# Performance work log

Measured on AMD Instinct MI355X. Metric: run time of the kernel, lower is better.

The kernel has to match this reference:

```python
import jax, jax.numpy as jnp
import numpy as np

B, C, H, W = 8, 256, 48, 48
EPS = 1e-5  # BatchNorm2d default eps


def setup_inputs() -> dict:
    key = jax.random.key(0)
    ks = jax.random.split(key, 8)
    return {
        "Q_feat_s": jax.random.normal(ks[0], (B, C, H, W), dtype=jnp.float32),
        "KV_feat_s": jax.random.normal(ks[1], (B, C, H, W), dtype=jnp.float32),
        "Wq": jax.random.normal(ks[2], (C, C), dtype=jnp.float32) * 0.02,
        "Wk": jax.random.normal(ks[3], (C, C), dtype=jnp.float32) * 0.02,
        "Wv": jax.random.normal(ks[4], (C, C), dtype=jnp.float32) * 0.02,
        "Wz": jax.random.normal(ks[5], (C, C), dtype=jnp.float32) * 0.02,
        "bn_gamma": jnp.ones((C,), dtype=jnp.float32),
        "bn_beta": jnp.zeros((C,), dtype=jnp.float32),
        "bn_mean": jax.random.normal(ks[6], (C,), dtype=jnp.float32) * 0.1,
        "bn_var": jax.random.uniform(ks[7], (C,), dtype=jnp.float32, minval=0.5, maxval=1.5),
    }


def reference(Q_feat_s, KV_feat_s, Wq, Wk, Wv, Wz, bn_gamma, bn_beta, bn_mean, bn_var):
    b, c, h, w = Q_feat_s.shape
    n = h * w
    # 1x1 convs == channel-mixing matmuls
    Q = jnp.einsum('oc,bchw->bohw', Wq, Q_feat_s).reshape(b, c, n)      # [B,C,N]
    K = jnp.einsum('oc,bchw->bohw', Wk, KV_feat_s).reshape(b, c, n)     # [B,C,N]
    V = jnp.einsum('oc,bchw->bohw', Wv, KV_feat_s).reshape(b, c, n)     # [B,C,N]
    # attn = (Q^T K)/N then @ V^T; linear (no softmax) so reassociate: Q^T (K V^T)/N
    KV = jnp.einsum('bcn,bdn->bcd', K, V) / n                           # [B,C,C]
    QKV = jnp.einsum('bcn,bcd->bdn', Q, KV)                             # [B,C,N]
    x = QKV.reshape(b, c, h, w)
    # W_z 1x1 conv + BatchNorm2d (inference / running stats)
    z = jnp.einsum('oc,bchw->bohw', Wz, x)
    inv = bn_gamma / jnp.sqrt(bn_var + EPS)
    z = z * inv[None, :, None, None] + (bn_beta - bn_mean * inv)[None, :, None, None]
    return z + Q_feat_s
```

## Files before the change

### kernel.cpp

```cpp
#include <hip/hip_runtime.h>

#define Bv 8
#define Cc 256
#define Nn 2304
#define EPS 1e-5f

typedef float f32x4 __attribute__((ext_vector_type(4)));
typedef __bf16 bf16x8 __attribute__((ext_vector_type(8)));

static __device__ __forceinline__ f32x4 mfma16(bf16x8 a, bf16x8 b, f32x4 c) {
    return __builtin_amdgcn_mfma_f32_16x16x32_bf16(a, b, c, 0, 0, 0);
}

static __device__ __forceinline__ bf16x8 load_cvt8(const float* __restrict__ p) {
    float4 a = *(const float4*)p;
    float4 b = *(const float4*)(p + 4);
    bf16x8 r;
    r[0] = (__bf16)a.x; r[1] = (__bf16)a.y; r[2] = (__bf16)a.z; r[3] = (__bf16)a.w;
    r[4] = (__bf16)b.x; r[5] = (__bf16)b.y; r[6] = (__bf16)b.z; r[7] = (__bf16)b.w;
    return r;
}

static __device__ __forceinline__ bf16x8 load_add_cvt8(const float* __restrict__ p0,
                                                       const float* __restrict__ p1) {
    float4 a0 = *(const float4*)p0;
    float4 a1 = *(const float4*)(p0 + 4);
    float4 b0 = *(const float4*)p1;
    float4 b1 = *(const float4*)(p1 + 4);
    bf16x8 r;
    r[0] = (__bf16)(a0.x + b0.x); r[1] = (__bf16)(a0.y + b0.y);
    r[2] = (__bf16)(a0.z + b0.z); r[3] = (__bf16)(a0.w + b0.w);
    r[4] = (__bf16)(a1.x + b1.x); r[5] = (__bf16)(a1.y + b1.y);
    r[6] = (__bf16)(a1.z + b1.z); r[7] = (__bf16)(a1.w + b1.w);
    return r;
}

__global__ __launch_bounds__(256) void k_fused1(
    const float* __restrict__ Qf, const float* __restrict__ KVf,
    const float* __restrict__ Wq, const float* __restrict__ Wk,
    const float* __restrict__ Wv, const float* __restrict__ Wz,
    const float* __restrict__ gamma, const float* __restrict__ var_,
    unsigned short* __restrict__ Lb_us, unsigned short* __restrict__ Rtb_us,
    unsigned short* __restrict__ Qft_us, float* __restrict__ Spart) {
    __shared__ __align__(16) char smem[32768];
    int blk = blockIdx.x, tid = threadIdx.x;

    if (blk < 256) {
        __bf16 (*As)[72] = (__bf16 (*)[72])smem;
        __bf16 (*Bs)[72] = (__bf16 (*)[72])(smem + 9216);
        int b = blk & 7;
        int tt = (blk >> 3) & 15;
        int kc = blk >> 7;
        int tr = (tt >> 2) * 64, tc = (tt & 3) * 64;
        int k0 = kc * 1152;
        int l = tid & 63, w = tid >> 6;
        int lr = l & 15, kofs = (l >> 4) * 8;
        int row = tid >> 2, c0 = (tid & 3) * 16;
        const float* Abase = KVf + ((size_t)b * Cc + tr) * Nn + k0;
        const float* Bbase = KVf + ((size_t)b * Cc + tc) * Nn + k0;
        f32x4 zero = {0.f, 0.f, 0.f, 0.f};
        f32x4 acc[4] = {zero, zero, zero, zero};
        for (int ks = 0; ks < 18; ++ks) {
            const float* ap = Abase + (size_t)row * Nn + ks * 64 + c0;
            const float* bp = Bbase + (size_t)row * Nn + ks * 64 + c0;
            *(bf16x8*)&As[row][c0]     = load_cvt8(ap);
            *(bf16x8*)&As[row][c0 + 8] = load_cvt8(ap + 8);
            *(bf16x8*)&Bs[row][c0]     = load_cvt8(bp);
            *(bf16x8*)&Bs[row][c0 + 8] = load_cvt8(bp + 8);
            __syncthreads();
#pragma unroll
            for (int kk = 0; kk < 64; kk += 32) {
                bf16x8 af = *(const bf16x8*)&As[w * 16 + lr][kk + kofs];
#pragma unroll
                for (int j = 0; j < 4; ++j) {
                    bf16x8 bb = *(const bf16x8*)&Bs[j * 16 + lr][kk + kofs];
                    acc[j] = mfma16(af, bb, acc[j]);
                }
            }
            __syncthreads();
        }
        float* Sp = Spart + ((size_t)kc * Bv + b) * 65536;
        int row0 = tr + w * 16 + ((l >> 4) << 2);
#pragma unroll
        for (int j = 0; j < 4; ++j) {
            int col = tc + j * 16 + lr;
#pragma unroll
            for (int r = 0; r < 4; ++r)
                Sp[(size_t)(row0 + r) * 256 + col] = acc[j][r];
        }
    } else if (blk < 768) {
        float* bufA = (float*)smem;
        float* bufB = bufA + 4096;
        __bf16* Lb  = (__bf16*)Lb_us;
        __bf16* Rtb = (__bf16*)Rtb_us;
        int wblk = blk - 256;
        bool isL = (wblk < 256);
        int t = isL ? wblk : wblk - 256;
        int tr = (t >> 4) * 16, tc = (t & 15) * 16;
        if (isL) {
            for (int idx = tid; idx < 4096; idx += 256) {
                int r = idx >> 8, m = idx & 255;
                bufA[idx] = Wz[(tr + r) * 256 + m];
            }
            for (int idx = tid; idx < 4096; idx += 256) {
                int m = idx >> 4, j = idx & 15;
                bufB[idx] = Wv[m * 256 + tc + j];
            }
        } else {
            for (int idx = tid; idx < 4096; idx += 256) {
                int o = idx >> 4, j = idx & 15;
                bufA[idx] = Wq[o * 256 + tr + j];
                bufB[idx] = Wk[o * 256 + tc + j];
            }
        }
        __syncthreads();
        int oo = tid >> 4, cc = tid & 15;
        float sum = 0.f;
        if (isL) {
#pragma unroll 8
            for (int m = 0; m < 256; ++m) sum += bufA[oo * 256 + m] * bufB[m * 16 + cc];
            int o = tr + oo;
            float inv = gamma[o] / sqrtf(var_[o] + EPS);
            Lb[o * 256 + tc + cc] = (__bf16)(inv * sum * (1.0f / (float)Nn));
        } else {
#pragma unroll 8
            for (int o = 0; o < 256; ++o) sum += bufA[o * 16 + oo] * bufB[o * 16 + cc];
            Rtb[(tr + oo) * 256 + tc + cc] = (__bf16)sum;
        }
    } else {
        float (*tile)[65] = (float (*)[65])smem;
        __bf16* Qft = (__bf16*)Qft_us;
        int t = blk - 768;
        int c0 = (t & 3) * 64;
        int u = t >> 2;
        int n0 = (u % 36) * 64;
        int b = u / 36;
        const float* src = Qf + (size_t)b * Cc * Nn;
        for (int idx = tid; idx < 4096; idx += 256) {
            int r = idx >> 6, cl = idx & 63;
            tile[r][cl] = src[(size_t)(c0 + r) * Nn + n0 + cl];
        }
        __syncthreads();
        __bf16* dst = Qft + ((size_t)b * Nn + n0) * 256 + c0;
        for (int idx = tid; idx < 4096; idx += 256) {
            int n = idx >> 6, c = idx & 63;
            dst[(size_t)n * 256 + c] = (__bf16)tile[c][n];
        }
    }
}

__global__ __launch_bounds__(256) void k_mid1(
    const unsigned short* __restrict__ Lb_us, const float* __restrict__ Spart,
    float* __restrict__ Tpart) {
    const __bf16* Lb = (const __bf16*)Lb_us;
    int blk = blockIdx.x;
    int b = blk & 7;
    int t = (blk >> 3) & 15;
    int kc = blk >> 7;
    int tr = (t >> 2) * 64, tc = (t & 3) * 64;
    int k0 = kc * 128;
    int tid = threadIdx.x, l = tid & 63, w = tid >> 6;
    int lr = l & 15, kofs = (l >> 4) * 8;
    const float* S0 = Spart + (size_t)b * 65536;
    const float* S1 = Spart + (size_t)(Bv + b) * 65536;
    f32x4 zero = {0.f, 0.f, 0.f, 0.f};
    f32x4 acc[4] = {zero, zero, zero, zero};
    int arow = tr + w * 16 + lr;
    for (int kk = 0; kk < 128; kk += 32) {
        bf16x8 af = *(const bf16x8*)&Lb[arow * 256 + k0 + kk + kofs];
#pragma unroll
        for (int j = 0; j < 4; ++j) {
            int brow = tc + j * 16 + lr;
            bf16x8 bb = load_add_cvt8(&S0[(size_t)brow * 256 + k0 + kk + kofs],
                                      &S1[(size_t)brow * 256 + k0 + kk + kofs]);
            acc[j] = mfma16(af, bb, acc[j]);
        }
    }
    float* Tp = Tpart + ((size_t)kc * Bv + b) * 65536;
    int row0 = tr + w * 16 + ((l >> 4) << 2);
#pragma unroll
    for (int j = 0; j < 4; ++j) {
        int col = tc + j * 16 + lr;
#pragma unroll
        for (int r = 0; r < 4; ++r)
            Tp[(size_t)(row0 + r) * 256 + col] = acc[j][r];
    }
}

__global__ __launch_bounds__(256) void k_mid2(
    const float* __restrict__ Tpart, const unsigned short* __restrict__ Rtb_us,
    unsigned short* __restrict__ Pb_us) {
    const __bf16* Rtb = (const __bf16*)Rtb_us;
    __bf16* Pb = (__bf16*)Pb_us;
    int blk = blockIdx.x;
    int b = blk & 7;
    int t = blk >> 3;
    int tr = (t >> 2) * 64, tc = (t & 3) * 64;
    int tid = threadIdx.x, l = tid & 63, w = tid >> 6;
    int lr = l & 15, kofs = (l >> 4) * 8;
    const float* T0 = Tpart + (size_t)b * 65536;
    const float* T1 = Tpart + (size_t)(Bv + b) * 65536;
    f32x4 zero = {0.f, 0.f, 0.f, 0.f};
    f32x4 acc[4] = {zero, zero, zero, zero};
    int arow = tr + w * 16 + lr;
    for (int kk = 0; kk < 256; kk += 32) {
        bf16x8 af = load_add_cvt8(&T0[(size_t)arow * 256 + kk + kofs],
                                  &T1[(size_t)arow * 256 + kk + kofs]);
#pragma unroll
        for (int j = 0; j < 4; ++j) {
            int brow = tc + j * 16 + lr;
            bf16x8 bb = *(const bf16x8*)&Rtb[brow * 256 + kk + kofs];
            acc[j] = mfma16(af, bb, acc[j]);
        }
    }
    __bf16* Pbb = Pb + ((size_t)b << 16);
    int row0 = tr + w * 16 + ((l >> 4) << 2);
#pragma unroll
    for (int j = 0; j < 4; ++j) {
        int col = tc + j * 16 + lr;
#pragma unroll
        for (int r = 0; r < 4; ++r)
            Pbb[(size_t)(row0 + r) * 256 + col] = (__bf16)acc[j][r];
    }
}

__global__ __launch_bounds__(512) void k_out(
    const unsigned short* __restrict__ Pb_us, const unsigned short* __restrict__ Qft_us,
    const float* __restrict__ Qf,
    const float* __restrict__ gamma, const float* __restrict__ beta,
    const float* __restrict__ mean, const float* __restrict__ var_,
    float* __restrict__ out) {
    const __bf16* Pb = (const __bf16*)Pb_us;
    const __bf16* Qft = (const __bf16*)Qft_us;
    int bid = blockIdx.x;
    int b = bid & 7, nt = bid >> 3;
    int tid = threadIdx.x, l = tid & 63, w = tid >> 6;
    int lr = l & 15, kofs = (l >> 4) * 8;
    int obase = w * 32;
    int nbase = nt * 64;
    const __bf16* A = Pb + ((size_t)b << 16);
    const __bf16* Bt = Qft + (size_t)b * Nn * 256;
    f32x4 zero = {0.f, 0.f, 0.f, 0.f};
    f32x4 acc[2][4];
#pragma unroll
    for (int i = 0; i < 2; ++i)
#pragma unroll
        for (int j = 0; j < 4; ++j) acc[i][j] = zero;

    for (int kk = 0; kk < 256; kk += 32) {
        bf16x8 af[2], bb[4];
#pragma unroll
        for (int i = 0; i < 2; ++i)
            af[i] = *(const bf16x8*)&A[(size_t)(obase + i * 16 + lr) * 256 + kk + kofs];
#pragma unroll
        for (int j = 0; j < 4; ++j)
            bb[j] = *(const bf16x8*)&Bt[(size_t)(nbase + j * 16 + lr) * 256 + kk + kofs];
#pragma unroll
        for (int i = 0; i < 2; ++i)
#pragma unroll
            for (int j = 0; j < 4; ++j)
                acc[i][j] = mfma16(af[i], bb[j], acc[i][j]);
    }

    const float* Qfb = Qf + (size_t)b * Cc * Nn;
    float* outb = out + (size_t)b * Cc * Nn;
#pragma unroll
    for (int i = 0; i < 2; ++i) {
        int o0 = obase + i * 16 + ((l >> 4) << 2);
#pragma unroll
        for (int r = 0; r < 4; ++r) {
            int o = o0 + r;
            float inv = gamma[o] / sqrtf(var_[o] + EPS);
            float shift = beta[o] - mean[o] * inv;
#pragma unroll
            for (int j = 0; j < 4; ++j) {
                int n = nbase + j * 16 + lr;
                outb[(size_t)o * Nn + n] = acc[i][j][r] + shift + Qfb[(size_t)o * Nn + n];
            }
        }
    }
}

extern "C" void kernel_launch(void* const* d_in, const int* in_sizes, int n_in,
                              void* d_out, int out_size, void* d_ws, size_t ws_size,
                              hipStream_t stream) {
    (void)in_sizes; (void)n_in; (void)out_size; (void)ws_size;
    const float* Qf    = (const float*)d_in[0];
    const float* KVf   = (const float*)d_in[1];
    const float* Wq    = (const float*)d_in[2];
    const float* Wk    = (const float*)d_in[3];
    const float* Wv    = (const float*)d_in[4];
    const float* Wz    = (const float*)d_in[5];
    const float* gamma = (const float*)d_in[6];
    const float* beta  = (const float*)d_in[7];
    const float* mean  = (const float*)d_in[8];
    const float* var_  = (const float*)d_in[9];
    float* out = (float*)d_out;

    char* ws = (char*)d_ws;
    float* Spart        = (float*)ws;
    float* Tpart        = (float*)(ws + (4u << 20));
    unsigned short* Lb  = (unsigned short*)(ws + (8u << 20));
    unsigned short* Rtb = (unsigned short*)(ws + (8u << 20) + (128u << 10));
    unsigned short* Pb  = (unsigned short*)(ws + (8u << 20) + (256u << 10));
    unsigned short* Qft = (unsigned short*)(ws + (9u << 20) + (256u << 10));

    k_fused1<<<1920, 256, 0, stream>>>(Qf, KVf, Wq, Wk, Wv, Wz, gamma, var_,
                                       Lb, Rtb, Qft, Spart);
    k_mid1<<<256, 256, 0, stream>>>(Lb, Spart, Tpart);
    k_mid2<<<128, 256, 0, stream>>>(Tpart, Rtb, Pb);
    k_out<<<288, 512, 0, stream>>>(Pb, Qft, Qf, gamma, beta, mean, var_, out);
}
```

Before: 165.3 us.

## Fuse Q transpose into output kernel, split Gram K-reduction four ways, prefetch tiles

Drops the separate Q-feature transpose/bf16 conversion stage and its workspace round-trip. The output GEMM kernel now loads the fp32 Q tile, converts it and transposes it into shared memory directly. The KV Gram computation is split into four K-chunks instead of two, doubling the block count for better occupancy, with register prefetch of the next tile overlapping the MFMA work. The mid kernel now sums four partials instead of two, which adds partial-buffer traffic. Shared-memory transposed stores in k_out may bank-conflict.

```diff
diff --git a/kernel.cpp b/kernel.cpp
--- a/kernel.cpp
+++ b/kernel.cpp
@@ -12,12 +12,33 @@
     return __builtin_amdgcn_mfma_f32_16x16x32_bf16(a, b, c, 0, 0, 0);
 }
 
-static __device__ __forceinline__ bf16x8 load_cvt8(const float* __restrict__ p) {
-    float4 a = *(const float4*)p;
-    float4 b = *(const float4*)(p + 4);
+static __device__ __forceinline__ bf16x8 cvt8(float4 a, float4 b) {
     bf16x8 r;
     r[0] = (__bf16)a.x; r[1] = (__bf16)a.y; r[2] = (__bf16)a.z; r[3] = (__bf16)a.w;
     r[4] = (__bf16)b.x; r[5] = (__bf16)b.y; r[6] = (__bf16)b.z; r[7] = (__bf16)b.w;
+    return r;
+}
+
+static __device__ __forceinline__ bf16x8 load_cvt8(const float* __restrict__ p) {
+    return cvt8(*(const float4*)p, *(const float4*)(p + 4));
+}
+
+static __device__ __forceinline__ bf16x8 load4_add_cvt8(
+    const float* __restrict__ p0, const float* __restrict__ p1,
+    const float* __restrict__ p2, const float* __restrict__ p3) {
+    float4 x0 = *(const float4*)p0, x1 = *(const float4*)(p0 + 4);
+    float4 y0 = *(const float4*)p1, y1 = *(const float4*)(p1 + 4);
+    float4 z0 = *(const float4*)p2, z1 = *(const float4*)(p2 + 4);
+    float4 w0 = *(const float4*)p3, w1 = *(const float4*)(p3 + 4);
+    bf16x8 r;
+    r[0] = (__bf16)(x0.x + y0.x + z0.x + w0.x);
+    r[1] = (__bf16)(x0.y + y0.y + z0.y + w0.y);
+    r[2] = (__bf16)(x0.z + y0.z + z0.z + w0.z);
+    r[3] = (__bf16)(x0.w + y0.w + z0.w + w0.w);
+    r[4] = (__bf16)(x1.x + y1.x + z1.x + w1.x);
+    r[5] = (__bf16)(x1.y + y1.y + z1.y + w1.y);
+    r[6] = (__bf16)(x1.z + y1.z + z1.z + w1.z);
+    r[7] = (__bf16)(x1.w + y1.w + z1.w + w1.w);
     return r;
 }
 
@@ -35,39 +56,48 @@
     return r;
 }
 
-__global__ __launch_bounds__(256) void k_fused1(
-    const float* __restrict__ Qf, const float* __restrict__ KVf,
+__global__ __launch_bounds__(256) void k_front(
+    const float* __restrict__ KVf,
     const float* __restrict__ Wq, const float* __restrict__ Wk,
     const float* __restrict__ Wv, const float* __restrict__ Wz,
     const float* __restrict__ gamma, const float* __restrict__ var_,
     unsigned short* __restrict__ Lb_us, unsigned short* __restrict__ Rtb_us,
-    unsigned short* __restrict__ Qft_us, float* __restrict__ Spart) {
+    float* __restrict__ Spart) {
     __shared__ __align__(16) char smem[32768];
     int blk = blockIdx.x, tid = threadIdx.x;
 
-    if (blk < 256) {
+    if (blk < 512) {
         __bf16 (*As)[72] = (__bf16 (*)[72])smem;
         __bf16 (*Bs)[72] = (__bf16 (*)[72])(smem + 9216);
         int b = blk & 7;
         int tt = (blk >> 3) & 15;
         int kc = blk >> 7;
         int tr = (tt >> 2) * 64, tc = (tt & 3) * 64;
-        int k0 = kc * 1152;
+        int k0 = kc * 576;
         int l = tid & 63, w = tid >> 6;
         int lr = l & 15, kofs = (l >> 4) * 8;
         int row = tid >> 2, c0 = (tid & 3) * 16;
-        const float* Abase = KVf + ((size_t)b * Cc + tr) * Nn + k0;
-        const float* Bbase = KVf + ((size_t)b * Cc + tc) * Nn + k0;
+        const float* Ap = KVf + ((size_t)b * Cc + tr + row) * Nn + k0 + c0;
+        const float* Bp = KVf + ((size_t)b * Cc + tc + row) * Nn + k0 + c0;
+        float4 fa0, fa1, fa2, fa3, fb0, fb1, fb2, fb3;
+#define LD_TILE(ks) do { \
+        const float* ap_ = Ap + (ks) * 64; \
+        const float* bp_ = Bp + (ks) * 64; \
+        fa0 = *(const float4*)ap_;         fa1 = *(const float4*)(ap_ + 4); \
+        fa2 = *(const float4*)(ap_ + 8);   fa3 = *(const float4*)(ap_ + 12); \
+        fb0 = *(const float4*)bp_;         fb1 = *(const float4*)(bp_ + 4); \
+        fb2 = *(const float4*)(bp_ + 8);   fb3 = *(const float4*)(bp_ + 12); \
+    } while (0)
         f32x4 zero = {0.f, 0.f, 0.f, 0.f};
         f32x4 acc[4] = {zero, zero, zero, zero};
-        for (int ks = 0; ks < 18; ++ks) {
-            const float* ap = Abase + (size_t)row * Nn + ks * 64 + c0;
-            const float* bp = Bbase + (size_t)row * Nn + ks * 64 + c0;
-            *(bf16x8*)&As[row][c0]     = load_cvt8(ap);
-            *(bf16x8*)&As[row][c0 + 8] = load_cvt8(ap + 8);
-            *(bf16x8*)&Bs[row][c0]     = load_cvt8(bp);
-            *(bf16x8*)&Bs[row][c0 + 8] = load_cvt8(bp + 8);
+        LD_TILE(0);
+        for (int ks = 0; ks < 9; ++ks) {
+            *(bf16x8*)&As[row][c0]     = cvt8(fa0, fa1);
+            *(bf16x8*)&As[row][c0 + 8] = cvt8(fa2, fa3);
+            *(bf16x8*)&Bs[row][c0]     = cvt8(fb0, fb1);
+            *(bf16x8*)&Bs[row][c0 + 8] = cvt8(fb2, fb3);
             __syncthreads();
+            if (ks < 8) LD_TILE(ks + 1);
 #pragma unroll
             for (int kk = 0; kk < 64; kk += 32) {
                 bf16x8 af = *(const bf16x8*)&As[w * 16 + lr][kk + kofs];
@@ -79,6 +109,7 @@
             }
             __syncthreads();
         }
+#undef LD_TILE
         float* Sp = Spart + ((size_t)kc * Bv + b) * 65536;
         int row0 = tr + w * 16 + ((l >> 4) << 2);
 #pragma unroll
@@ -88,12 +119,12 @@
             for (int r = 0; r < 4; ++r)
                 Sp[(size_t)(row0 + r) * 256 + col] = acc[j][r];
         }
-    } else if (blk < 768) {
+    } else {
         float* bufA = (float*)smem;
         float* bufB = bufA + 4096;
         __bf16* Lb  = (__bf16*)Lb_us;
         __bf16* Rtb = (__bf16*)Rtb_us;
-        int wblk = blk - 256;
+        int wblk = blk - 512;
         bool isL = (wblk < 256);
         int t = isL ? wblk : wblk - 256;
         int tr = (t >> 4) * 16, tc = (t & 15) * 16;
@@ -127,25 +158,6 @@
             for (int o = 0; o < 256; ++o) sum += bufA[o * 16 + oo] * bufB[o * 16 + cc];
             Rtb[(tr + oo) * 256 + tc + cc] = (__bf16)sum;
         }
-    } else {
-        float (*tile)[65] = (float (*)[65])smem;
-        __bf16* Qft = (__bf16*)Qft_us;
-        int t = blk - 768;
-        int c0 = (t & 3) * 64;
-        int u = t >> 2;
-        int n0 = (u % 36) * 64;
-        int b = u / 36;
-        const float* src = Qf + (size_t)b * Cc * Nn;
-        for (int idx = tid; idx < 4096; idx += 256) {
-            int r = idx >> 6, cl = idx & 63;
-            tile[r][cl] = src[(size_t)(c0 + r) * Nn + n0 + cl];
-        }
-        __syncthreads();
-        __bf16* dst = Qft + ((size_t)b * Nn + n0) * 256 + c0;
-        for (int idx = tid; idx < 4096; idx += 256) {
-            int n = idx >> 6, c = idx & 63;
-            dst[(size_t)n * 256 + c] = (__bf16)tile[c][n];
-        }
     }
 }
 
@@ -161,8 +173,10 @@
     int k0 = kc * 128;
     int tid = threadIdx.x, l = tid & 63, w = tid >> 6;
     int lr = l & 15, kofs = (l >> 4) * 8;
-    const float* S0 = Spart + (size_t)b * 65536;
-    const float* S1 = Spart + (size_t)(Bv + b) * 65536;
+    const float* S0 = Spart + (size_t)(0 * Bv + b) * 65536;
+    const float* S1 = Spart + (size_t)(1 * Bv + b) * 65536;
+    const float* S2 = Spart + (size_t)(2 * Bv + b) * 65536;
+    const float* S3 = Spart + (size_t)(3 * Bv + b) * 65536;
     f32x4 zero = {0.f, 0.f, 0.f, 0.f};
     f32x4 acc[4] = {zero, zero, zero, zero};
     int arow = tr + w * 16 + lr;
@@ -170,9 +184,8 @@
         bf16x8 af = *(const bf16x8*)&Lb[arow * 256 + k0 + kk + kofs];
 #pragma unroll
         for (int j = 0; j < 4; ++j) {
-            int brow = tc + j * 16 + lr;
-            bf16x8 bb = load_add_cvt8(&S0[(size_t)brow * 256 + k0 + kk + kofs],
-                                      &S1[(size_t)brow * 256 + k0 + kk + kofs]);
+            size_t boff = (size_t)(tc + j * 16 + lr) * 256 + k0 + kk + kofs;
+            bf16x8 bb = load4_add_cvt8(S0 + boff, S1 + boff, S2 + boff, S3 + boff);
             acc[j] = mfma16(af, bb, acc[j]);
         }
     }
@@ -225,21 +238,31 @@
 }
 
 __global__ __launch_bounds__(512) void k_out(
-    const unsigned short* __restrict__ Pb_us, const unsigned short* __restrict__ Qft_us,
-    const float* __restrict__ Qf,
+    const unsigned short* __restrict__ Pb_us, const float* __restrict__ Qf,
     const float* __restrict__ gamma, const float* __restrict__ beta,
     const float* __restrict__ mean, const float* __restrict__ var_,
     float* __restrict__ out) {
+    __shared__ __bf16 Qs[64][264];
     const __bf16* Pb = (const __bf16*)Pb_us;
-    const __bf16* Qft = (const __bf16*)Qft_us;
     int bid = blockIdx.x;
     int b = bid & 7, nt = bid >> 3;
+    int n0 = nt * 64;
     int tid = threadIdx.x, l = tid & 63, w = tid >> 6;
     int lr = l & 15, kofs = (l >> 4) * 8;
+
+    const float* src = Qf + (size_t)b * Cc * Nn + n0;
+    for (int idx = tid; idx < 4096; idx += 512) {
+        int c = idx >> 4, ng = (idx & 15) << 2;
+        float4 v = *(const float4*)(src + (size_t)c * Nn + ng);
+        Qs[ng + 0][c] = (__bf16)v.x;
+        Qs[ng + 1][c] = (__bf16)v.y;
+        Qs[ng + 2][c] = (__bf16)v.z;
+        Qs[ng + 3][c] = (__bf16)v.w;
+    }
+    __syncthreads();
+
     int obase = w * 32;
-    int nbase = nt * 64;
     const __bf16* A = Pb + ((size_t)b << 16);
-    const __bf16* Bt = Qft + (size_t)b * Nn * 256;
     f32x4 zero = {0.f, 0.f, 0.f, 0.f};
     f32x4 acc[2][4];
 #pragma unroll
@@ -254,7 +277,7 @@
             af[i] = *(const bf16x8*)&A[(size_t)(obase + i * 16 + lr) * 256 + kk + kofs];
 #pragma unroll
         for (int j = 0; j < 4; ++j)
-            bb[j] = *(const bf16x8*)&Bt[(size_t)(nbase + j * 16 + lr) * 256 + kk + kofs];
+            bb[j] = *(const bf16x8*)&Qs[j * 16 + lr][kk + kofs];
 #pragma unroll
         for (int i = 0; i < 2; ++i)
 #pragma unroll
@@ -274,7 +297,7 @@
             float shift = beta[o] - mean[o] * inv;
 #pragma unroll
             for (int j = 0; j < 4; ++j) {
-                int n = nbase + j * 16 + lr;
+                int n = n0 + j * 16 + lr;
                 outb[(size_t)o * Nn + n] = acc[i][j][r] + shift + Qfb[(size_t)o * Nn + n];
             }
         }
@@ -299,15 +322,14 @@
 
     char* ws = (char*)d_ws;
     float* Spart        = (float*)ws;
-    float* Tpart        = (float*)(ws + (4u << 20));
-    unsigned short* Lb  = (unsigned short*)(ws + (8u << 20));
-    unsigned short* Rtb = (unsigned short*)(ws + (8u << 20) + (128u << 10));
-    unsigned short* Pb  = (unsigned short*)(ws + (8u << 20) + (256u << 10));
-    unsigned short* Qft = (unsigned short*)(ws + (9u << 20) + (256u << 10));
-
-    k_fused1<<<1920, 256, 0, stream>>>(Qf, KVf, Wq, Wk, Wv, Wz, gamma, var_,
-                                       Lb, Rtb, Qft, Spart);
+    float* Tpart        = (float*)(ws + (8u << 20));
+    unsigned short* Lb  = (unsigned short*)(ws + (12u << 20));
+    unsigned short* Rtb = (unsigned short*)(ws + (12u << 20) + (128u << 10));
+    unsigned short* Pb  = (unsigned short*)(ws + (12u << 20) + (256u << 10));
+
+    k_front<<<1024, 256, 0, stream>>>(KVf, Wq, Wk, Wv, Wz, gamma, var_,
+                                      Lb, Rtb, Spart);
     k_mid1<<<256, 256, 0, stream>>>(Lb, Spart, Tpart);
     k_mid2<<<128, 256, 0, stream>>>(Tpart, Rtb, Pb);
-    k_out<<<288, 512, 0, stream>>>(Pb, Qft, Qf, gamma, beta, mean, var_, out);
-}
+    k_out<<<288, 512, 0, stream>>>(Pb, Qf, gamma, beta, mean, var_, out);
+}
```

Result: faster. 156.5 us (median of 2 runs) (-5.3%).
